# Optimization experiments

Hardware: AMD Instinct MI355X
Metric: run time of the kernel (lower is better)

The kernel has to match this reference:

```python
import jax, jax.numpy as jnp
import numpy as np

D_MODEL = 768
D_INNER = 1536
D_STATE = 16
D_CONV = 4
DT_RANK = 48
N_LAYERS = 24
VOCAB = 50280
T_STEPS = 100
BATCH = 2
SEQ = 256


def _time_embeds():
    pos = np.arange(T_STEPS, dtype=np.float32)[:, None]
    i = np.arange(D_MODEL, dtype=np.float32)[None, :]
    angle_rates = 1.0 / np.power(10.0, (np.floor(i / 2) * 2) / D_MODEL)
    angles = pos * angle_rates
    pc = np.zeros_like(angles)
    pc[:, 0::2] = np.sin(angles[:, 0::2])
    pc[:, 1::2] = np.cos(angles[:, 1::2])
    return jnp.asarray(pc, dtype=jnp.float32)


def setup_inputs() -> dict:
    key = jax.random.key(0)
    ks = jax.random.split(key, 14)
    rn = lambda k, shape, s=0.02: (jax.random.normal(k, shape, jnp.float32) * s)
    inp = {}
    inp["states"] = jax.random.normal(ks[0], (3, BATCH, D_INNER, D_STATE), jnp.float32)
    inp["timesteps"] = jax.random.randint(ks[1], (BATCH,), 0, T_STEPS)
    inp["input_ids"] = jax.random.randint(ks[2], (BATCH, SEQ), 0, VOCAB)
    inp["time_embeds"] = _time_embeds()
    inp["embed"] = rn(ks[3], (VOCAB, D_MODEL))
    inp["norm_w"] = jnp.ones((N_LAYERS, D_MODEL), jnp.float32)
    inp["in_proj_w"] = rn(ks[4], (N_LAYERS, 2 * D_INNER, D_MODEL))
    inp["conv_w"] = rn(ks[5], (N_LAYERS, D_INNER, D_CONV), 0.1)
    inp["conv_b"] = rn(ks[6], (N_LAYERS, D_INNER), 0.1)
    inp["x_proj_w"] = rn(ks[7], (N_LAYERS, DT_RANK + 2 * D_STATE, D_INNER))
    inp["dt_proj_w"] = rn(ks[8], (N_LAYERS, D_INNER, DT_RANK))
    inp["dt_proj_b"] = rn(ks[9], (N_LAYERS, D_INNER), 0.5)
    inp["A_log"] = jnp.log(jnp.broadcast_to(jnp.arange(1, D_STATE + 1, dtype=jnp.float32), (N_LAYERS, D_INNER, D_STATE)))
    inp["D_skip"] = jnp.ones((N_LAYERS, D_INNER), jnp.float32)
    inp["out_proj_w"] = rn(ks[10], (N_LAYERS, D_MODEL, D_INNER))
    return inp


def _rms_norm(x, w, eps=1e-5):
    var = jnp.mean(x * x, axis=-1, keepdims=True)
    return x * jax.lax.rsqrt(var + eps) * w


def _mamba_layer(h, h0, norm_w, in_w, conv_w, conv_b, x_w, dt_w, dt_b, A_log, Dp, out_w):
    # h: [B, L, d_model]; h0: [B, d_inner, d_state] initial SSM state
    x = _rms_norm(h, norm_w)
    xz = jnp.einsum('bld,od->blo', x, in_w)           # [B, L, 2*d_inner]
    xc, z = jnp.split(xz, 2, axis=-1)
    # causal depthwise conv, kernel D_CONV, left-pad D_CONV-1
    xc_t = xc.transpose(0, 2, 1)                      # [B, d_inner, L]
    conv = jax.lax.conv_general_dilated(
        xc_t, conv_w[:, None, :], (1,), [(D_CONV - 1, 0)],
        feature_group_count=D_INNER, dimension_numbers=('NCH', 'OIH', 'NCH'))
    u = jax.nn.silu(conv + conv_b[None, :, None]).transpose(0, 2, 1)  # [B, L, d_inner]
    dbc = jnp.einsum('bld,od->blo', u, x_w)           # [B, L, dt_rank + 2*d_state]
    dt_low = dbc[..., :DT_RANK]
    Bm = dbc[..., DT_RANK:DT_RANK + D_STATE]          # [B, L, d_state]
    Cm = dbc[..., DT_RANK + D_STATE:]                 # [B, L, d_state]
    dt = jax.nn.softplus(jnp.einsum('blr,dr->bld', dt_low, dt_w) + dt_b)
    A = -jnp.exp(A_log)                               # [d_inner, d_state]
    dA = jnp.exp(dt[..., None] * A)                   # [B, L, d_inner, d_state]
    dBu = dt[..., None] * Bm[:, :, None, :] * u[..., None]

    def step(hc, inputs):
        dA_t, dBu_t, C_t = inputs
        hc = dA_t * hc + dBu_t                        # [B, d_inner, d_state]
        return hc, jnp.einsum('bds,bs->bd', hc, C_t)

    hL, ys = jax.lax.scan(step, h0, (dA.transpose(1, 0, 2, 3),
                                     dBu.transpose(1, 0, 2, 3),
                                     Cm.transpose(1, 0, 2)))
    y = ys.transpose(1, 0, 2) + Dp * u
    y = y * jax.nn.silu(z)
    return h + jnp.einsum('bld,od->blo', y, out_w), hL


def reference(states, timesteps, input_ids, time_embeds, embed, norm_w, in_proj_w,
              conv_w, conv_b, x_proj_w, dt_proj_w, dt_proj_b, A_log, D_skip, out_proj_w):
    h = embed[input_ids]                              # [B, L, d_model]
    z0 = jnp.zeros((h.shape[0], D_INNER, D_STATE), h.dtype)
    for l in range(21):
        h, _ = _mamba_layer(h, z0, norm_w[l], in_proj_w[l], conv_w[l], conv_b[l],
                            x_proj_w[l], dt_proj_w[l], dt_proj_b[l], A_log[l],
                            D_skip[l], out_proj_w[l])
    h = h + time_embeds[timesteps][:, None, :]
    last_states = []
    for l in range(21, 24):
        h, hl = _mamba_layer(h, states[l - 21], norm_w[l], in_proj_w[l], conv_w[l],
                             conv_b[l], x_proj_w[l], dt_proj_w[l], dt_proj_b[l],
                             A_log[l], D_skip[l], out_proj_w[l])
        last_states.append(hl)
    return jnp.stack(last_states)                     # [3, B, d_inner, d_state]
```

## Files before the change

kernel.cpp:

```cpp
#include <hip/hip_runtime.h>
#include <math.h>

#define D_MODEL 768
#define D_INNER 1536
#define D_STATE 16
#define DT_RANK 48
#define NLAYERS 24
#define BATCH 2
#define SEQ 256
#define M_ROWS (BATCH*SEQ)
#define DBC_COLS (DT_RANK + 2*D_STATE)

typedef __bf16 bf16x8 __attribute__((ext_vector_type(8)));
typedef float f32x4 __attribute__((ext_vector_type(4)));

__device__ __forceinline__ float siluf(float x) {
    return x / (1.0f + __expf(-x));
}

__global__ __launch_bounds__(256) void gather_kernel(const int* __restrict__ ids,
        const float* __restrict__ embed, float* __restrict__ h) {
    int m = blockIdx.x;
    long id = ids[m];
    const float* src = embed + id * D_MODEL;
    float* dst = h + m * D_MODEL;
    for (int k = threadIdx.x; k < D_MODEL; k += 256) dst[k] = src[k];
}

__global__ __launch_bounds__(256) void rmsnorm_kernel(const float* __restrict__ h,
        const float* __restrict__ w, float* __restrict__ x) {
    int m = blockIdx.x;
    const float* row = h + m * D_MODEL;
    float v[3];
    float ss = 0.f;
    #pragma unroll
    for (int i = 0; i < 3; ++i) {
        v[i] = row[threadIdx.x + i * 256];
        ss += v[i] * v[i];
    }
    #pragma unroll
    for (int off = 32; off > 0; off >>= 1) ss += __shfl_down(ss, off);
    __shared__ float wsum[4];
    int lane = threadIdx.x & 63, wid = threadIdx.x >> 6;
    if (lane == 0) wsum[wid] = ss;
    __syncthreads();
    float tot = wsum[0] + wsum[1] + wsum[2] + wsum[3];
    float inv = rsqrtf(tot / (float)D_MODEL + 1e-5f);
    float* xrow = x + m * D_MODEL;
    #pragma unroll
    for (int i = 0; i < 3; ++i) {
        int k = threadIdx.x + i * 256;
        xrow[k] = v[i] * inv * w[k];
    }
}

__global__ __launch_bounds__(256) void gemm_nt_mfma(const float* __restrict__ A,
        const float* __restrict__ B, float* __restrict__ C,
        int M, int N, int K, int lda, int ldb,
        const float* __restrict__ bias, int epi, int kchunk) {
    __shared__ __align__(16) __bf16 Ah[64][32];
    __shared__ __align__(16) __bf16 Al[64][32];
    __shared__ __align__(16) __bf16 Bh[64][32];
    __shared__ __align__(16) __bf16 Bl[64][32];
    const int t = threadIdx.x;
    const int m0 = blockIdx.y * 64, n0 = blockIdx.x * 64;
    const int kbeg = blockIdx.z * kchunk;
    const int kend = min(K, kbeg + kchunk);
    const int srow = t >> 2;
    const int skof = (t & 3) * 8;
    const int lane = t & 63;
    const int w = t >> 6;
    const int wm = (w >> 1) * 32, wn = (w & 1) * 32;
    const int lr = lane & 15, lg = lane >> 4;
    f32x4 acc[2][2] = {};
    const float* Ap0 = A + (size_t)(m0 + srow) * lda + skof;
    const bool nv = (n0 + srow) < N;
    const float* Bp0 = nv ? (B + (size_t)(n0 + srow) * ldb + skof) : A;
    for (int k0 = kbeg; k0 < kend; k0 += 32) {
        float va[8];
        if (k0 + skof + 8 <= kend) {
            float4 p = *(const float4*)(Ap0 + k0);
            float4 q = *(const float4*)(Ap0 + k0 + 4);
            va[0] = p.x; va[1] = p.y; va[2] = p.z; va[3] = p.w;
            va[4] = q.x; va[5] = q.y; va[6] = q.z; va[7] = q.w;
        } else {
            #pragma unroll
            for (int j = 0; j < 8; ++j)
                va[j] = (k0 + skof + j < kend) ? Ap0[k0 + j] : 0.f;
        }
        {
            bf16x8 hv, lv;
            #pragma unroll
            for (int j = 0; j < 8; ++j) {
                __bf16 hb = (__bf16)va[j];
                hv[j] = hb;
                lv[j] = (__bf16)(va[j] - (float)hb);
            }
            *reinterpret_cast<bf16x8*>(&Ah[srow][skof]) = hv;
            *reinterpret_cast<bf16x8*>(&Al[srow][skof]) = lv;
        }
        float vb[8];
        if (nv) {
            if (k0 + skof + 8 <= kend) {
                float4 p = *(const float4*)(Bp0 + k0);
                float4 q = *(const float4*)(Bp0 + k0 + 4);
                vb[0] = p.x; vb[1] = p.y; vb[2] = p.z; vb[3] = p.w;
                vb[4] = q.x; vb[5] = q.y; vb[6] = q.z; vb[7] = q.w;
            } else {
                #pragma unroll
                for (int j = 0; j < 8; ++j)
                    vb[j] = (k0 + skof + j < kend) ? Bp0[k0 + j] : 0.f;
            }
        } else {
            #pragma unroll
            for (int j = 0; j < 8; ++j) vb[j] = 0.f;
        }
        {
            bf16x8 hv, lv;
            #pragma unroll
            for (int j = 0; j < 8; ++j) {
                __bf16 hb = (__bf16)vb[j];
                hv[j] = hb;
                lv[j] = (__bf16)(vb[j] - (float)hb);
            }
            *reinterpret_cast<bf16x8*>(&Bh[srow][skof]) = hv;
            *reinterpret_cast<bf16x8*>(&Bl[srow][skof]) = lv;
        }
        __syncthreads();
        bf16x8 ah[2], al[2], bh[2], bl[2];
        #pragma unroll
        for (int mi = 0; mi < 2; ++mi) {
            ah[mi] = *reinterpret_cast<const bf16x8*>(&Ah[wm + mi * 16 + lr][lg * 8]);
            al[mi] = *reinterpret_cast<const bf16x8*>(&Al[wm + mi * 16 + lr][lg * 8]);
        }
        #pragma unroll
        for (int ni = 0; ni < 2; ++ni) {
            bh[ni] = *reinterpret_cast<const bf16x8*>(&Bh[wn + ni * 16 + lr][lg * 8]);
            bl[ni] = *reinterpret_cast<const bf16x8*>(&Bl[wn + ni * 16 + lr][lg * 8]);
        }
        #pragma unroll
        for (int mi = 0; mi < 2; ++mi) {
            #pragma unroll
            for (int ni = 0; ni < 2; ++ni) {
                acc[mi][ni] = __builtin_amdgcn_mfma_f32_16x16x32_bf16(ah[mi], bh[ni], acc[mi][ni], 0, 0, 0);
                acc[mi][ni] = __builtin_amdgcn_mfma_f32_16x16x32_bf16(al[mi], bh[ni], acc[mi][ni], 0, 0, 0);
                acc[mi][ni] = __builtin_amdgcn_mfma_f32_16x16x32_bf16(ah[mi], bl[ni], acc[mi][ni], 0, 0, 0);
                acc[mi][ni] = __builtin_amdgcn_mfma_f32_16x16x32_bf16(al[mi], bl[ni], acc[mi][ni], 0, 0, 0);
            }
        }
        __syncthreads();
    }
    float* Cz = C + (gridDim.z > 1 ? (size_t)blockIdx.z * M * N : 0);
    #pragma unroll
    for (int mi = 0; mi < 2; ++mi) {
        #pragma unroll
        for (int ni = 0; ni < 2; ++ni) {
            int n = n0 + wn + ni * 16 + lr;
            if (n < N) {
                #pragma unroll
                for (int r = 0; r < 4; ++r) {
                    int m = m0 + wm + mi * 16 + lg * 4 + r;
                    float vv = acc[mi][ni][r];
                    if (epi == 1) {
                        vv += bias[n];
                        vv = vv > 20.f ? vv : log1pf(expf(vv));
                    }
                    Cz[(size_t)m * N + n] = vv;
                }
            }
        }
    }
}

__global__ __launch_bounds__(256) void reduce_splitk(const float* __restrict__ P,
        float* __restrict__ C, int MN, int accum) {
    int i = blockIdx.x * 256 + threadIdx.x;
    if (i < MN) {
        float v = P[i] + P[MN + i] + P[2 * MN + i] + P[3 * MN + i];
        if (accum) C[i] += v; else C[i] = v;
    }
}

__global__ __launch_bounds__(256) void conv_silu_kernel(const float* __restrict__ xz,
        const float* __restrict__ w, const float* __restrict__ cb,
        float* __restrict__ u) {
    int g = blockIdx.x * 256 + threadIdx.x;
    int d = g % D_INNER;
    int m = g / D_INNER;
    int l = m % SEQ;
    int b = m / SEQ;
    float acc = cb[d];
    #pragma unroll
    for (int j = 0; j < 4; ++j) {
        int ll = l - 3 + j;
        if (ll >= 0)
            acc += xz[(long)(b * SEQ + ll) * (2 * D_INNER) + d] * w[d * 4 + j];
    }
    u[(long)m * D_INNER + d] = siluf(acc);
}

#define SCAN_TILE 64
__global__ __launch_bounds__(256) void scan_kernel(const float* __restrict__ dt,
        const float* __restrict__ u, const float* __restrict__ dbc,
        const float* __restrict__ xz, const float* __restrict__ A_log,
        const float* __restrict__ Dskip, const float* __restrict__ h0,
        float* __restrict__ y, float* __restrict__ outstate) {
    __shared__ float sdt[SCAN_TILE][16];
    __shared__ float su [SCAN_TILE][16];
    __shared__ float sz [SCAN_TILE][16];
    __shared__ float sBC[SCAN_TILE][32];
    __shared__ float sy [SCAN_TILE][16];
    int t = threadIdx.x;
    int s = t & 15;
    int pair = t >> 4;
    int gp = blockIdx.x * 16 + pair;
    int b = gp / D_INNER;
    int d = gp % D_INNER;
    int d0 = (blockIdx.x * 16) % D_INNER;
    float A_s = -__expf(A_log[d * D_STATE + s]);
    float hst = h0 ? h0[(size_t)(b * D_INNER + d) * D_STATE + s] : 0.0f;
    float Dv = Dskip[d];
    for (int l0 = 0; l0 < SEQ; l0 += SCAN_TILE) {
        #pragma unroll
        for (int k = 0; k < 4; ++k) {
            int idx = t + k * 256;
            int l = idx >> 4, j = idx & 15;
            size_t m = (size_t)(b * SEQ + l0 + l);
            sdt[l][j] = dt[m * D_INNER + d0 + j];
            su [l][j] = u [m * D_INNER + d0 + j];
            float zv  = xz[m * (2 * D_INNER) + D_INNER + d0 + j];
            sz [l][j] = siluf(zv);
        }
        #pragma unroll
        for (int k = 0; k < 8; ++k) {
            int idx = t + k * 256;
            int l = idx >> 5, c = idx & 31;
            size_t m = (size_t)(b * SEQ + l0 + l);
            sBC[l][c] = dbc[m * DBC_COLS + DT_RANK + c];
        }
        __syncthreads();
        #pragma unroll 4
        for (int l = 0; l < SCAN_TILE; ++l) {
            float dtv = sdt[l][pair];
            float uv  = su [l][pair];
            float Bv  = sBC[l][s];
            float Cv  = sBC[l][16 + s];
            float dA = __expf(dtv * A_s);
            hst = dA * hst + dtv * Bv * uv;
            float p = hst * Cv;
            p += __shfl_xor(p, 1);
            p += __shfl_xor(p, 2);
            p += __shfl_xor(p, 4);
            p += __shfl_xor(p, 8);
            if (s == 0) sy[l][pair] = (p + Dv * uv) * sz[l][pair];
        }
        __syncthreads();
        #pragma unroll
        for (int k = 0; k < 4; ++k) {
            int idx = t + k * 256;
            int l = idx >> 4, j = idx & 15;
            size_t m = (size_t)(b * SEQ + l0 + l);
            y[m * D_INNER + d0 + j] = sy[l][j];
        }
    }
    if (outstate) outstate[(size_t)(b * D_INNER + d) * D_STATE + s] = hst;
}

__global__ __launch_bounds__(256) void add_time_kernel(float* __restrict__ h,
        const float* __restrict__ te, const int* __restrict__ ts) {
    int g = blockIdx.x * 256 + threadIdx.x;
    int m = g / D_MODEL;
    int k = g - m * D_MODEL;
    int b = m / SEQ;
    h[g] += te[(long)ts[b] * D_MODEL + k];
}

extern "C" void kernel_launch(void* const* d_in, const int* in_sizes, int n_in,
                              void* d_out, int out_size, void* d_ws, size_t ws_size,
                              hipStream_t stream) {
    const float* states     = (const float*)d_in[0];
    const int*   timesteps  = (const int*)d_in[1];
    const int*   input_ids  = (const int*)d_in[2];
    const float* time_emb   = (const float*)d_in[3];
    const float* embed      = (const float*)d_in[4];
    const float* norm_w     = (const float*)d_in[5];
    const float* in_proj_w  = (const float*)d_in[6];
    const float* conv_w     = (const float*)d_in[7];
    const float* conv_b     = (const float*)d_in[8];
    const float* x_proj_w   = (const float*)d_in[9];
    const float* dt_proj_w  = (const float*)d_in[10];
    const float* dt_proj_b  = (const float*)d_in[11];
    const float* A_log      = (const float*)d_in[12];
    const float* D_skip     = (const float*)d_in[13];
    const float* out_proj_w = (const float*)d_in[14];
    float* out = (float*)d_out;

    float* h   = (float*)d_ws;
    float* x   = h   + M_ROWS * D_MODEL;
    float* xz  = x   + M_ROWS * D_MODEL;
    float* u   = xz  + M_ROWS * 2 * D_INNER;
    float* dbc = u   + M_ROWS * D_INNER;
    float* dt  = dbc + M_ROWS * DBC_COLS;
    float* y   = dt  + M_ROWS * D_INNER;
    float* px  = x;
    float* po  = u;

    gather_kernel<<<M_ROWS, 256, 0, stream>>>(input_ids, embed, h);

    for (int l = 0; l < NLAYERS; ++l) {
        const float* nw  = norm_w     + (size_t)l * D_MODEL;
        const float* iw  = in_proj_w  + (size_t)l * 2 * D_INNER * D_MODEL;
        const float* cw  = conv_w     + (size_t)l * D_INNER * 4;
        const float* cb  = conv_b     + (size_t)l * D_INNER;
        const float* xw  = x_proj_w   + (size_t)l * DBC_COLS * D_INNER;
        const float* dw  = dt_proj_w  + (size_t)l * D_INNER * DT_RANK;
        const float* db  = dt_proj_b  + (size_t)l * D_INNER;
        const float* al  = A_log      + (size_t)l * D_INNER * D_STATE;
        const float* dsk = D_skip     + (size_t)l * D_INNER;
        const float* ow  = out_proj_w + (size_t)l * D_MODEL * D_INNER;

        rmsnorm_kernel<<<M_ROWS, 256, 0, stream>>>(h, nw, x);

        gemm_nt_mfma<<<dim3(2 * D_INNER / 64, M_ROWS / 64, 1), 256, 0, stream>>>(
            x, iw, xz, M_ROWS, 2 * D_INNER, D_MODEL, D_MODEL, D_MODEL, nullptr, 0, D_MODEL);

        conv_silu_kernel<<<M_ROWS * D_INNER / 256, 256, 0, stream>>>(xz, cw, cb, u);

        gemm_nt_mfma<<<dim3(2, M_ROWS / 64, 4), 256, 0, stream>>>(
            u, xw, px, M_ROWS, DBC_COLS, D_INNER, D_INNER, D_INNER, nullptr, 0, D_INNER / 4);
        reduce_splitk<<<(M_ROWS * DBC_COLS + 255) / 256, 256, 0, stream>>>(
            px, dbc, M_ROWS * DBC_COLS, 0);

        gemm_nt_mfma<<<dim3(D_INNER / 64, M_ROWS / 64, 1), 256, 0, stream>>>(
            dbc, dw, dt, M_ROWS, D_INNER, DT_RANK, DBC_COLS, DT_RANK, db, 1, DT_RANK);

        const float* h0  = (l >= 21) ? states + (size_t)(l - 21) * BATCH * D_INNER * D_STATE : nullptr;
        float* ostate    = (l >= 21) ? out + (size_t)(l - 21) * BATCH * D_INNER * D_STATE : nullptr;
        scan_kernel<<<BATCH * D_INNER / 16, 256, 0, stream>>>(
            dt, u, dbc, xz, al, dsk, h0, y, ostate);

        gemm_nt_mfma<<<dim3(D_MODEL / 64, M_ROWS / 64, 4), 256, 0, stream>>>(
            y, ow, po, M_ROWS, D_MODEL, D_INNER, D_INNER, D_INNER, nullptr, 0, D_INNER / 4);
        reduce_splitk<<<(M_ROWS * D_MODEL + 255) / 256, 256, 0, stream>>>(
            po, h, M_ROWS * D_MODEL, 1);

        if (l == 20) {
            add_time_kernel<<<M_ROWS * D_MODEL / 256, 256, 0, stream>>>(h, time_emb, timesteps);
        }
    }
}
```

Before: 4.507 ms.

## Pre-split operands to bf16 hi/lo, async LDS loads, drop lo*lo MFMA term

Weights are split once per call into padded bf16 hi/lo arrays, and activations are split by the producing kernels (rmsnorm, conv, reduce, scan), so the GEMM no longer converts fp32 inside its inner loop. The GEMM now uses global_load_lds with double-buffered, swizzled LDS and 64x128 tiles. It also drops the lo*lo MFMA, cutting MFMA work by a quarter at a small accuracy cost. The trade-off is a large workspace and an extra weight-split pass on every call.

```diff
diff --git a/kernel.cpp b/kernel.cpp
--- a/kernel.cpp
+++ b/kernel.cpp
@@ -13,9 +13,17 @@
 
 typedef __bf16 bf16x8 __attribute__((ext_vector_type(8)));
 typedef float f32x4 __attribute__((ext_vector_type(4)));
+typedef unsigned int u32;
+#define AS1 __attribute__((address_space(1)))
+#define AS3 __attribute__((address_space(3)))
 
 __device__ __forceinline__ float siluf(float x) {
     return x / (1.0f + __expf(-x));
+}
+__device__ __forceinline__ void split1(float v, __bf16* hp, __bf16* lp) {
+    __bf16 hb = (__bf16)v;
+    *hp = hb;
+    *lp = (__bf16)(v - (float)hb);
 }
 
 __global__ __launch_bounds__(256) void gather_kernel(const int* __restrict__ ids,
@@ -27,8 +35,49 @@
     for (int k = threadIdx.x; k < D_MODEL; k += 256) dst[k] = src[k];
 }
 
+__global__ __launch_bounds__(256) void split8_kernel(const float* __restrict__ src,
+        __bf16* __restrict__ hi, __bf16* __restrict__ lo, long n8) {
+    long i = (long)blockIdx.x * 256 + threadIdx.x;
+    if (i >= n8) return;
+    const float4* s = (const float4*)(src + i * 8);
+    float4 p = s[0], q = s[1];
+    float v[8] = {p.x, p.y, p.z, p.w, q.x, q.y, q.z, q.w};
+    bf16x8 hv, lv;
+    #pragma unroll
+    for (int j = 0; j < 8; ++j) {
+        __bf16 hb = (__bf16)v[j];
+        hv[j] = hb;
+        lv[j] = (__bf16)(v[j] - (float)hb);
+    }
+    *(bf16x8*)(hi + i * 8) = hv;
+    *(bf16x8*)(lo + i * 8) = lv;
+}
+
+__global__ __launch_bounds__(256) void padsplit_x(const float* __restrict__ src,
+        __bf16* __restrict__ hi, __bf16* __restrict__ lo) {
+    long i = (long)blockIdx.x * 256 + threadIdx.x;
+    if (i >= 24L * 128 * 1536) return;
+    long c = i % 1536;
+    long rl = i / 1536;
+    int row = (int)(rl % 128);
+    int l = (int)(rl / 128);
+    float v = (row < DBC_COLS) ? src[((long)l * DBC_COLS + row) * 1536 + c] : 0.f;
+    split1(v, hi + i, lo + i);
+}
+
+__global__ __launch_bounds__(256) void padsplit_dt(const float* __restrict__ src,
+        __bf16* __restrict__ hi, __bf16* __restrict__ lo) {
+    long i = (long)blockIdx.x * 256 + threadIdx.x;
+    if (i >= 24L * 1536 * 64) return;
+    int c = (int)(i % 64);
+    long r = (i / 64) % 1536;
+    int l = (int)(i / (64L * 1536));
+    float v = (c < DT_RANK) ? src[((long)l * 1536 + r) * DT_RANK + c] : 0.f;
+    split1(v, hi + i, lo + i);
+}
+
 __global__ __launch_bounds__(256) void rmsnorm_kernel(const float* __restrict__ h,
-        const float* __restrict__ w, float* __restrict__ x) {
+        const float* __restrict__ w, __bf16* __restrict__ xh, __bf16* __restrict__ xl) {
     int m = blockIdx.x;
     const float* row = h + m * D_MODEL;
     float v[3];
@@ -46,123 +95,108 @@
     __syncthreads();
     float tot = wsum[0] + wsum[1] + wsum[2] + wsum[3];
     float inv = rsqrtf(tot / (float)D_MODEL + 1e-5f);
-    float* xrow = x + m * D_MODEL;
     #pragma unroll
     for (int i = 0; i < 3; ++i) {
         int k = threadIdx.x + i * 256;
-        xrow[k] = v[i] * inv * w[k];
-    }
-}
-
-__global__ __launch_bounds__(256) void gemm_nt_mfma(const float* __restrict__ A,
-        const float* __restrict__ B, float* __restrict__ C,
-        int M, int N, int K, int lda, int ldb,
+        float o = v[i] * inv * w[k];
+        split1(o, xh + m * D_MODEL + k, xl + m * D_MODEL + k);
+    }
+}
+
+#define LDSBUF 24576
+__global__ __launch_bounds__(256) void gemm_bf16s(
+        const __bf16* __restrict__ Ah, const __bf16* __restrict__ Al, int lda,
+        const __bf16* __restrict__ Bh, const __bf16* __restrict__ Bl, int ldb,
+        float* __restrict__ C, int M, int N,
         const float* __restrict__ bias, int epi, int kchunk) {
-    __shared__ __align__(16) __bf16 Ah[64][32];
-    __shared__ __align__(16) __bf16 Al[64][32];
-    __shared__ __align__(16) __bf16 Bh[64][32];
-    __shared__ __align__(16) __bf16 Bl[64][32];
+    __shared__ __align__(16) __bf16 smem[2 * LDSBUF / 2];
     const int t = threadIdx.x;
-    const int m0 = blockIdx.y * 64, n0 = blockIdx.x * 64;
+    const int lane = t & 63, w = t >> 6;
+    const int m0 = blockIdx.y * 64, n0 = blockIdx.x * 128;
     const int kbeg = blockIdx.z * kchunk;
-    const int kend = min(K, kbeg + kchunk);
-    const int srow = t >> 2;
-    const int skof = (t & 3) * 8;
-    const int lane = t & 63;
-    const int w = t >> 6;
-    const int wm = (w >> 1) * 32, wn = (w & 1) * 32;
+    const int wm = (w & 1) * 32, wn = (w >> 1) * 64;
     const int lr = lane & 15, lg = lane >> 4;
-    f32x4 acc[2][2] = {};
-    const float* Ap0 = A + (size_t)(m0 + srow) * lda + skof;
-    const bool nv = (n0 + srow) < N;
-    const float* Bp0 = nv ? (B + (size_t)(n0 + srow) * ldb + skof) : A;
-    for (int k0 = kbeg; k0 < kend; k0 += 32) {
-        float va[8];
-        if (k0 + skof + 8 <= kend) {
-            float4 p = *(const float4*)(Ap0 + k0);
-            float4 q = *(const float4*)(Ap0 + k0 + 4);
-            va[0] = p.x; va[1] = p.y; va[2] = p.z; va[3] = p.w;
-            va[4] = q.x; va[5] = q.y; va[6] = q.z; va[7] = q.w;
-        } else {
+    const int swz = ((lg ^ ((lr >> 1) & 3)) << 4);
+    const int srow = lane >> 2;
+    const int scg = (lane & 3) ^ ((lane >> 3) & 3);
+    const __bf16* gsrc[6];
+    int loff[6];
+    #pragma unroll
+    for (int i = 0; i < 6; ++i) {
+        int id = w * 6 + i;
+        int arr = (id < 4) ? 0 : (id < 8) ? 1 : (id < 16) ? 2 : 3;
+        int rowbase = (arr < 2) ? ((id & 3) << 4) : ((id & 7) << 4);
+        const __bf16* base;
+        int ld, r0, arroff;
+        if (arr == 0)      { base = Ah; ld = lda; r0 = m0; arroff = 0; }
+        else if (arr == 1) { base = Al; ld = lda; r0 = m0; arroff = 4096; }
+        else if (arr == 2) { base = Bh; ld = ldb; r0 = n0; arroff = 8192; }
+        else               { base = Bl; ld = ldb; r0 = n0; arroff = 16384; }
+        gsrc[i] = base + (size_t)(r0 + rowbase + srow) * ld + kbeg + scg * 8;
+        loff[i] = arroff + rowbase * 64;
+    }
+    f32x4 acc[2][4] = {};
+    const int nsteps = kchunk / 32;
+
+    #pragma unroll
+    for (int i = 0; i < 6; ++i) {
+        __builtin_amdgcn_global_load_lds(
+            (const AS1 u32*)(const void*)gsrc[i],
+            (AS3 u32*)(void*)((char*)smem + loff[i]), 16, 0, 0);
+    }
+    __syncthreads();
+    int cur = 0;
+    for (int s = 0; s < nsteps; ++s) {
+        if (s + 1 < nsteps) {
+            int koff = (s + 1) * 32;
+            int bufoff = (cur ^ 1) * LDSBUF;
             #pragma unroll
-            for (int j = 0; j < 8; ++j)
-                va[j] = (k0 + skof + j < kend) ? Ap0[k0 + j] : 0.f;
-        }
-        {
-            bf16x8 hv, lv;
-            #pragma unroll
-            for (int j = 0; j < 8; ++j) {
-                __bf16 hb = (__bf16)va[j];
-                hv[j] = hb;
-                lv[j] = (__bf16)(va[j] - (float)hb);
+            for (int i = 0; i < 6; ++i) {
+                __builtin_amdgcn_global_load_lds(
+                    (const AS1 u32*)(const void*)(gsrc[i] + koff),
+                    (AS3 u32*)(void*)((char*)smem + bufoff + loff[i]), 16, 0, 0);
             }
-            *reinterpret_cast<bf16x8*>(&Ah[srow][skof]) = hv;
-            *reinterpret_cast<bf16x8*>(&Al[srow][skof]) = lv;
-        }
-        float vb[8];
-        if (nv) {
-            if (k0 + skof + 8 <= kend) {
-                float4 p = *(const float4*)(Bp0 + k0);
-                float4 q = *(const float4*)(Bp0 + k0 + 4);
-                vb[0] = p.x; vb[1] = p.y; vb[2] = p.z; vb[3] = p.w;
-                vb[4] = q.x; vb[5] = q.y; vb[6] = q.z; vb[7] = q.w;
-            } else {
-                #pragma unroll
-                for (int j = 0; j < 8; ++j)
-                    vb[j] = (k0 + skof + j < kend) ? Bp0[k0 + j] : 0.f;
-            }
-        } else {
-            #pragma unroll
-            for (int j = 0; j < 8; ++j) vb[j] = 0.f;
-        }
-        {
-            bf16x8 hv, lv;
-            #pragma unroll
-            for (int j = 0; j < 8; ++j) {
-                __bf16 hb = (__bf16)vb[j];
-                hv[j] = hb;
-                lv[j] = (__bf16)(vb[j] - (float)hb);
-            }
-            *reinterpret_cast<bf16x8*>(&Bh[srow][skof]) = hv;
-            *reinterpret_cast<bf16x8*>(&Bl[srow][skof]) = lv;
-        }
-        __syncthreads();
-        bf16x8 ah[2], al[2], bh[2], bl[2];
+        }
+        const char* sb = (const char*)smem + cur * LDSBUF;
+        bf16x8 ah[2], al[2], bh[4], bl[4];
         #pragma unroll
         for (int mi = 0; mi < 2; ++mi) {
-            ah[mi] = *reinterpret_cast<const bf16x8*>(&Ah[wm + mi * 16 + lr][lg * 8]);
-            al[mi] = *reinterpret_cast<const bf16x8*>(&Al[wm + mi * 16 + lr][lg * 8]);
-        }
-        #pragma unroll
-        for (int ni = 0; ni < 2; ++ni) {
-            bh[ni] = *reinterpret_cast<const bf16x8*>(&Bh[wn + ni * 16 + lr][lg * 8]);
-            bl[ni] = *reinterpret_cast<const bf16x8*>(&Bl[wn + ni * 16 + lr][lg * 8]);
+            int r = wm + mi * 16 + lr;
+            ah[mi] = *(const bf16x8*)(sb + r * 64 + swz);
+            al[mi] = *(const bf16x8*)(sb + 4096 + r * 64 + swz);
+        }
+        #pragma unroll
+        for (int ni = 0; ni < 4; ++ni) {
+            int r = wn + ni * 16 + lr;
+            bh[ni] = *(const bf16x8*)(sb + 8192 + r * 64 + swz);
+            bl[ni] = *(const bf16x8*)(sb + 16384 + r * 64 + swz);
         }
         #pragma unroll
         for (int mi = 0; mi < 2; ++mi) {
             #pragma unroll
-            for (int ni = 0; ni < 2; ++ni) {
+            for (int ni = 0; ni < 4; ++ni) {
                 acc[mi][ni] = __builtin_amdgcn_mfma_f32_16x16x32_bf16(ah[mi], bh[ni], acc[mi][ni], 0, 0, 0);
+                acc[mi][ni] = __builtin_amdgcn_mfma_f32_16x16x32_bf16(ah[mi], bl[ni], acc[mi][ni], 0, 0, 0);
                 acc[mi][ni] = __builtin_amdgcn_mfma_f32_16x16x32_bf16(al[mi], bh[ni], acc[mi][ni], 0, 0, 0);
-                acc[mi][ni] = __builtin_amdgcn_mfma_f32_16x16x32_bf16(ah[mi], bl[ni], acc[mi][ni], 0, 0, 0);
-                acc[mi][ni] = __builtin_amdgcn_mfma_f32_16x16x32_bf16(al[mi], bl[ni], acc[mi][ni], 0, 0, 0);
             }
         }
         __syncthreads();
-    }
-    float* Cz = C + (gridDim.z > 1 ? (size_t)blockIdx.z * M * N : 0);
-    #pragma unroll
-    for (int mi = 0; mi < 2; ++mi) {
-        #pragma unroll
-        for (int ni = 0; ni < 2; ++ni) {
-            int n = n0 + wn + ni * 16 + lr;
-            if (n < N) {
+        cur ^= 1;
+    }
+    float* Cz = C + (size_t)blockIdx.z * M * N;
+    #pragma unroll
+    for (int ni = 0; ni < 4; ++ni) {
+        int n = n0 + wn + ni * 16 + lr;
+        if (n < N) {
+            float bv = (epi == 1) ? bias[n] : 0.f;
+            #pragma unroll
+            for (int mi = 0; mi < 2; ++mi) {
                 #pragma unroll
                 for (int r = 0; r < 4; ++r) {
                     int m = m0 + wm + mi * 16 + lg * 4 + r;
                     float vv = acc[mi][ni][r];
                     if (epi == 1) {
-                        vv += bias[n];
+                        vv += bv;
                         vv = vv > 20.f ? vv : log1pf(expf(vv));
                     }
                     Cz[(size_t)m * N + n] = vv;
@@ -173,17 +207,34 @@
 }
 
 __global__ __launch_bounds__(256) void reduce_splitk(const float* __restrict__ P,
-        float* __restrict__ C, int MN, int accum) {
+        float* __restrict__ C, int MN, int Z, int accum) {
     int i = blockIdx.x * 256 + threadIdx.x;
     if (i < MN) {
-        float v = P[i] + P[MN + i] + P[2 * MN + i] + P[3 * MN + i];
+        float v = 0.f;
+        for (int z = 0; z < Z; ++z) v += P[(size_t)z * MN + i];
         if (accum) C[i] += v; else C[i] = v;
+    }
+}
+
+__global__ __launch_bounds__(256) void reduce_dbc(const float* __restrict__ P,
+        float* __restrict__ dbc, __bf16* __restrict__ dh, __bf16* __restrict__ dl) {
+    int i = blockIdx.x * 256 + threadIdx.x;
+    const int MN = M_ROWS * DBC_COLS;
+    if (i >= MN) return;
+    float v = 0.f;
+    #pragma unroll
+    for (int z = 0; z < 8; ++z) v += P[(size_t)z * MN + i];
+    dbc[i] = v;
+    int m = i / DBC_COLS, c = i - m * DBC_COLS;
+    if (c < 64) {
+        float vv = (c < DT_RANK) ? v : 0.f;
+        split1(vv, dh + m * 64 + c, dl + m * 64 + c);
     }
 }
 
 __global__ __launch_bounds__(256) void conv_silu_kernel(const float* __restrict__ xz,
         const float* __restrict__ w, const float* __restrict__ cb,
-        float* __restrict__ u) {
+        float* __restrict__ u, __bf16* __restrict__ uh, __bf16* __restrict__ ul) {
     int g = blockIdx.x * 256 + threadIdx.x;
     int d = g % D_INNER;
     int m = g / D_INNER;
@@ -196,7 +247,10 @@
         if (ll >= 0)
             acc += xz[(long)(b * SEQ + ll) * (2 * D_INNER) + d] * w[d * 4 + j];
     }
-    u[(long)m * D_INNER + d] = siluf(acc);
+    float uv = siluf(acc);
+    long o = (long)m * D_INNER + d;
+    u[o] = uv;
+    split1(uv, uh + o, ul + o);
 }
 
 #define SCAN_TILE 64
@@ -204,7 +258,8 @@
         const float* __restrict__ u, const float* __restrict__ dbc,
         const float* __restrict__ xz, const float* __restrict__ A_log,
         const float* __restrict__ Dskip, const float* __restrict__ h0,
-        float* __restrict__ y, float* __restrict__ outstate) {
+        __bf16* __restrict__ yh, __bf16* __restrict__ yl,
+        float* __restrict__ outstate) {
     __shared__ float sdt[SCAN_TILE][16];
     __shared__ float su [SCAN_TILE][16];
     __shared__ float sz [SCAN_TILE][16];
@@ -260,7 +315,7 @@
             int idx = t + k * 256;
             int l = idx >> 4, j = idx & 15;
             size_t m = (size_t)(b * SEQ + l0 + l);
-            y[m * D_INNER + d0 + j] = sy[l][j];
+            split1(sy[l][j], yh + m * D_INNER + d0 + j, yl + m * D_INNER + d0 + j);
         }
     }
     if (outstate) outstate[(size_t)(b * D_INNER + d) * D_STATE + s] = hst;
@@ -295,54 +350,84 @@
     const float* out_proj_w = (const float*)d_in[14];
     float* out = (float*)d_out;
 
-    float* h   = (float*)d_ws;
-    float* x   = h   + M_ROWS * D_MODEL;
-    float* xz  = x   + M_ROWS * D_MODEL;
-    float* u   = xz  + M_ROWS * 2 * D_INNER;
-    float* dbc = u   + M_ROWS * D_INNER;
-    float* dt  = dbc + M_ROWS * DBC_COLS;
-    float* y   = dt  + M_ROWS * D_INNER;
-    float* px  = x;
-    float* po  = u;
+    float* h    = (float*)d_ws;
+    float* xz   = h    + M_ROWS * D_MODEL;
+    float* u    = xz   + M_ROWS * 2 * D_INNER;
+    float* dbcf = u    + M_ROWS * D_INNER;
+    float* dtf  = dbcf + M_ROWS * DBC_COLS;
+    float* px   = dtf  + M_ROWS * D_INNER;
+    float* po   = px   + 8 * M_ROWS * DBC_COLS;
+    __bf16* bp  = (__bf16*)(po + 4 * M_ROWS * D_MODEL);
+    __bf16* xh = bp;               bp += M_ROWS * D_MODEL;
+    __bf16* xl = bp;               bp += M_ROWS * D_MODEL;
+    __bf16* uh = bp;               bp += M_ROWS * D_INNER;
+    __bf16* ul = bp;               bp += M_ROWS * D_INNER;
+    __bf16* yh = bp;               bp += M_ROWS * D_INNER;
+    __bf16* yl = bp;               bp += M_ROWS * D_INNER;
+    __bf16* dbh = bp;              bp += M_ROWS * 64;
+    __bf16* dbl_ = bp;             bp += M_ROWS * 64;
+    const long IN_W = 24L * 2 * D_INNER * D_MODEL;
+    const long OUT_W = 24L * D_MODEL * D_INNER;
+    const long X_W  = 24L * 128 * D_INNER;
+    const long DT_W = 24L * D_INNER * 64;
+    __bf16* wih = bp;              bp += IN_W;
+    __bf16* wil = bp;              bp += IN_W;
+    __bf16* woh = bp;              bp += OUT_W;
+    __bf16* wol = bp;              bp += OUT_W;
+    __bf16* wxh = bp;              bp += X_W;
+    __bf16* wxl = bp;              bp += X_W;
+    __bf16* wdh = bp;              bp += DT_W;
+    __bf16* wdl = bp;              bp += DT_W;
 
     gather_kernel<<<M_ROWS, 256, 0, stream>>>(input_ids, embed, h);
 
+    split8_kernel<<<(int)(IN_W / 8 / 256), 256, 0, stream>>>(in_proj_w, wih, wil, IN_W / 8);
+    split8_kernel<<<(int)(OUT_W / 8 / 256), 256, 0, stream>>>(out_proj_w, woh, wol, OUT_W / 8);
+    padsplit_x<<<(int)(X_W / 256), 256, 0, stream>>>(x_proj_w, wxh, wxl);
+    padsplit_dt<<<(int)(DT_W / 256), 256, 0, stream>>>(dt_proj_w, wdh, wdl);
+
     for (int l = 0; l < NLAYERS; ++l) {
-        const float* nw  = norm_w     + (size_t)l * D_MODEL;
-        const float* iw  = in_proj_w  + (size_t)l * 2 * D_INNER * D_MODEL;
-        const float* cw  = conv_w     + (size_t)l * D_INNER * 4;
-        const float* cb  = conv_b     + (size_t)l * D_INNER;
-        const float* xw  = x_proj_w   + (size_t)l * DBC_COLS * D_INNER;
-        const float* dw  = dt_proj_w  + (size_t)l * D_INNER * DT_RANK;
-        const float* db  = dt_proj_b  + (size_t)l * D_INNER;
-        const float* al  = A_log      + (size_t)l * D_INNER * D_STATE;
-        const float* dsk = D_skip     + (size_t)l * D_INNER;
-        const float* ow  = out_proj_w + (size_t)l * D_MODEL * D_INNER;
-
-        rmsnorm_kernel<<<M_ROWS, 256, 0, stream>>>(h, nw, x);
-
-        gemm_nt_mfma<<<dim3(2 * D_INNER / 64, M_ROWS / 64, 1), 256, 0, stream>>>(
-            x, iw, xz, M_ROWS, 2 * D_INNER, D_MODEL, D_MODEL, D_MODEL, nullptr, 0, D_MODEL);
-
-        conv_silu_kernel<<<M_ROWS * D_INNER / 256, 256, 0, stream>>>(xz, cw, cb, u);
-
-        gemm_nt_mfma<<<dim3(2, M_ROWS / 64, 4), 256, 0, stream>>>(
-            u, xw, px, M_ROWS, DBC_COLS, D_INNER, D_INNER, D_INNER, nullptr, 0, D_INNER / 4);
-        reduce_splitk<<<(M_ROWS * DBC_COLS + 255) / 256, 256, 0, stream>>>(
-            px, dbc, M_ROWS * DBC_COLS, 0);
-
-        gemm_nt_mfma<<<dim3(D_INNER / 64, M_ROWS / 64, 1), 256, 0, stream>>>(
-            dbc, dw, dt, M_ROWS, D_INNER, DT_RANK, DBC_COLS, DT_RANK, db, 1, DT_RANK);
+        const float* nw  = norm_w    + (size_t)l * D_MODEL;
+        const float* cw  = conv_w    + (size_t)l * D_INNER * 4;
+        const float* cb  = conv_b    + (size_t)l * D_INNER;
+        const float* db  = dt_proj_b + (size_t)l * D_INNER;
+        const float* al  = A_log     + (size_t)l * D_INNER * D_STATE;
+        const float* dsk = D_skip    + (size_t)l * D_INNER;
+        const __bf16* lwih = wih + (size_t)l * 2 * D_INNER * D_MODEL;
+        const __bf16* lwil = wil + (size_t)l * 2 * D_INNER * D_MODEL;
+        const __bf16* lwoh = woh + (size_t)l * D_MODEL * D_INNER;
+        const __bf16* lwol = wol + (size_t)l * D_MODEL * D_INNER;
+        const __bf16* lwxh = wxh + (size_t)l * 128 * D_INNER;
+        const __bf16* lwxl = wxl + (size_t)l * 128 * D_INNER;
+        const __bf16* lwdh = wdh + (size_t)l * D_INNER * 64;
+        const __bf16* lwdl = wdl + (size_t)l * D_INNER * 64;
+
+        rmsnorm_kernel<<<M_ROWS, 256, 0, stream>>>(h, nw, xh, xl);
+
+        gemm_bf16s<<<dim3(2 * D_INNER / 128, M_ROWS / 64, 1), 256, 0, stream>>>(
+            xh, xl, D_MODEL, lwih, lwil, D_MODEL, xz, M_ROWS, 2 * D_INNER,
+            nullptr, 0, D_MODEL);
+
+        conv_silu_kernel<<<M_ROWS * D_INNER / 256, 256, 0, stream>>>(xz, cw, cb, u, uh, ul);
+
+        gemm_bf16s<<<dim3(1, M_ROWS / 64, 8), 256, 0, stream>>>(
+            uh, ul, D_INNER, lwxh, lwxl, D_INNER, px, M_ROWS, DBC_COLS,
+            nullptr, 0, D_INNER / 8);
+        reduce_dbc<<<(M_ROWS * DBC_COLS + 255) / 256, 256, 0, stream>>>(px, dbcf, dbh, dbl_);
+
+        gemm_bf16s<<<dim3(D_INNER / 128, M_ROWS / 64, 1), 256, 0, stream>>>(
+            dbh, dbl_, 64, lwdh, lwdl, 64, dtf, M_ROWS, D_INNER, db, 1, 64);
 
         const float* h0  = (l >= 21) ? states + (size_t)(l - 21) * BATCH * D_INNER * D_STATE : nullptr;
         float* ostate    = (l >= 21) ? out + (size_t)(l - 21) * BATCH * D_INNER * D_STATE : nullptr;
         scan_kernel<<<BATCH * D_INNER / 16, 256, 0, stream>>>(
-            dt, u, dbc, xz, al, dsk, h0, y, ostate);
-
-        gemm_nt_mfma<<<dim3(D_MODEL / 64, M_ROWS / 64, 4), 256, 0, stream>>>(
-            y, ow, po, M_ROWS, D_MODEL, D_INNER, D_INNER, D_INNER, nullptr, 0, D_INNER / 4);
+            dtf, u, dbcf, xz, al, dsk, h0, yh, yl, ostate);
+
+        gemm_bf16s<<<dim3(D_MODEL / 128, M_ROWS / 64, 4), 256, 0, stream>>>(
+            yh, yl, D_INNER, lwoh, lwol, D_INNER, po, M_ROWS, D_MODEL,
+            nullptr, 0, D_INNER / 4);
         reduce_splitk<<<(M_ROWS * D_MODEL + 255) / 256, 256, 0, stream>>>(
-            po, h, M_ROWS * D_MODEL, 1);
+            po, h, M_ROWS * D_MODEL, 4, 1);
 
         if (l == 20) {
             add_time_kernel<<<M_ROWS * D_MODEL / 256, 256, 0, stream>>>(h, time_emb, timesteps);
```

New measurement: 4.141 ms. 8.1% less time.
